# Optimization experiments

Measured on AMD Instinct MI355X. Metric: run time of the kernel, lower is better.

The kernel has to match this reference:

```python
import jax, jax.numpy as jnp
import numpy as np

EPS = 1e-12


def sage_pool_conv(x, src, dst, W_pool, b_pool, W_self, W_neigh, b, num_nodes):
    """DGL SAGEConv with aggregator_type='pool':
    h_neigh[v] = max_{u in N(v)} relu(x[u] @ W_pool + b_pool)
    out[v] = x[v] @ W_self + h_neigh[v] @ W_neigh + b
    Zero-in-degree nodes get h_neigh = 0 (DGL fills max over empty set with 0).
    """
    m = jax.nn.relu(x[src] @ W_pool + b_pool)            # [E, F] gathered + transformed
    agg = jax.ops.segment_max(m, dst, num_segments=num_nodes)  # [N, F], -inf where no neighbors
    agg = jnp.where(jnp.isneginf(agg), 0.0, agg)
    return x @ W_self + agg @ W_neigh + b


def l2norm_relu(h):
    # F.normalize(h, p=2, dim=1, eps=1e-12) then relu
    n = jnp.maximum(jnp.linalg.norm(h, axis=1, keepdims=True), EPS)
    return jax.nn.relu(h / n)


def setup_inputs() -> dict:
    key = jax.random.key(0)
    N, E = 50000, 1600000
    IN, HID, OUT = 128, 128, 128
    ks = jax.random.split(key, 16)
    s = 0.05
    return {
        "x": jax.random.normal(ks[0], (N, IN), dtype=jnp.float32),
        "src": jax.random.randint(ks[1], (E,), 0, N, dtype=jnp.int32),
        "dst": jax.random.randint(ks[2], (E,), 0, N, dtype=jnp.int32),
        "W_pool1": jax.random.normal(ks[3], (IN, IN), dtype=jnp.float32) * s,
        "b_pool1": jnp.zeros((IN,), dtype=jnp.float32),
        "W_self1": jax.random.normal(ks[4], (IN, HID), dtype=jnp.float32) * s,
        "W_neigh1": jax.random.normal(ks[5], (IN, HID), dtype=jnp.float32) * s,
        "b1": jnp.zeros((HID,), dtype=jnp.float32),
        "W_pool2": jax.random.normal(ks[6], (HID, HID), dtype=jnp.float32) * s,
        "b_pool2": jnp.zeros((HID,), dtype=jnp.float32),
        "W_self2": jax.random.normal(ks[7], (HID, OUT), dtype=jnp.float32) * s,
        "W_neigh2": jax.random.normal(ks[8], (HID, OUT), dtype=jnp.float32) * s,
        "b2": jnp.zeros((OUT,), dtype=jnp.float32),
    }


def reference(x, src, dst, W_pool1, b_pool1, W_self1, W_neigh1, b1,
              W_pool2, b_pool2, W_self2, W_neigh2, b2):
    N = x.shape[0]
    h = sage_pool_conv(x, src, dst, W_pool1, b_pool1, W_self1, W_neigh1, b1, N)
    h = l2norm_relu(h)
    # dropout_1 is re-assigned in the original forward but never applied -> no dropout
    h = sage_pool_conv(h, src, dst, W_pool2, b_pool2, W_self2, W_neigh2, b2, N)
    h = l2norm_relu(h)
    return h
```

## Files before the change

### kernel.cpp

```cpp
#include <hip/hip_runtime.h>
#include <hip/hip_bf16.h>

#define NF 128

typedef __attribute__((ext_vector_type(8))) short bf8;
typedef __attribute__((ext_vector_type(4))) float f4;
typedef unsigned short u16x8 __attribute__((ext_vector_type(8)));

static __device__ __forceinline__ unsigned short f2bf(float f) {
  unsigned u = __builtin_bit_cast(unsigned, f);
  u = u + 0x7FFF + ((u >> 16) & 1);
  return (unsigned short)(u >> 16);
}

static __device__ __forceinline__ uint4 pkmax4(uint4 a, uint4 b) {
  u16x8 x = __builtin_bit_cast(u16x8, a);
  u16x8 y = __builtin_bit_cast(u16x8, b);
  u16x8 m = __builtin_elementwise_max(x, y);
  return __builtin_bit_cast(uint4, m);
}

static __device__ __forceinline__ uint4 shflxor4(uint4 a, int m) {
  uint4 r;
  r.x = (unsigned)__shfl_xor((int)a.x, m, 64);
  r.y = (unsigned)__shfl_xor((int)a.y, m, 64);
  r.z = (unsigned)__shfl_xor((int)a.z, m, 64);
  r.w = (unsigned)__shfl_xor((int)a.w, m, 64);
  return r;
}


__global__ void k_convX(const float* __restrict__ A, unsigned short* __restrict__ B,
                        long long nelem, int* __restrict__ bcnt, int nb) {
  long long i = (long long)(blockIdx.x * blockDim.x + threadIdx.x) * 8;
  if (blockIdx.x == 0 && (int)threadIdx.x < nb) bcnt[threadIdx.x] = 0;
  if (i + 8 > nelem) return;
  float4 a = *(const float4*)(A + i);
  float4 b = *(const float4*)(A + i + 4);
  uint4 o;
  o.x = f2bf(a.x) | ((unsigned)f2bf(a.y) << 16);
  o.y = f2bf(a.z) | ((unsigned)f2bf(a.w) << 16);
  o.z = f2bf(b.x) | ((unsigned)f2bf(b.y) << 16);
  o.w = f2bf(b.z) | ((unsigned)f2bf(b.w) << 16);
  *(uint4*)(B + i) = o;
}


__global__ void k_packW(const float* W0, const float* W1, const float* W2,
                        const float* W3, const float* W4, const float* W5,
                        unsigned short* __restrict__ out) {
  int gid = blockIdx.x * blockDim.x + threadIdx.x;
  int m = gid >> 11;
  int u = gid & 2047;
  if (m >= 6) return;
  const float* W = (m == 0) ? W0 : (m == 1) ? W1 : (m == 2) ? W2
                 : (m == 3) ? W3 : (m == 4) ? W4 : W5;
  int l = u & 63, c = u >> 6;
  int kk = c & 3, t = c >> 2;
  int kb = kk * 32 + ((l >> 4) << 3);
  int n = t * 16 + (l & 15);
  unsigned short* o = out + (size_t)m * 2048 * 8 + (size_t)u * 8;
  #pragma unroll
  for (int j = 0; j < 8; ++j) o[j] = f2bf(W[(size_t)(kb + j) * NF + n]);
}


#define TILE_B 8192

__global__ __launch_bounds__(256) void k_bhist(const int* __restrict__ dst,
                                               int* __restrict__ bcnt, int E) {
  __shared__ int h[256];
  int tid = threadIdx.x;
  h[tid] = 0;
  __syncthreads();
  int t0 = blockIdx.x * TILE_B;
  int tend = min(E, t0 + TILE_B);
  for (int i = t0 + tid; i < tend; i += 256) atomicAdd(&h[dst[i] >> 8], 1);
  __syncthreads();
  if (h[tid] > 0) atomicAdd(&bcnt[tid], h[tid]);
}

__global__ __launch_bounds__(256) void k_bscan(const int* __restrict__ bcnt,
                                               int* __restrict__ boff,
                                               int* __restrict__ cursors,
                                               int* __restrict__ off,
                                               int nb, int N, int E) {
  __shared__ int sc[256];
  int tid = threadIdx.x;
  int v = (tid < nb) ? bcnt[tid] : 0;
  sc[tid] = v;
  __syncthreads();
  for (int d = 1; d < 256; d <<= 1) {
    int t = (tid >= d) ? sc[tid - d] : 0;
    __syncthreads();
    sc[tid] += t;
    __syncthreads();
  }
  if (tid < nb) {
    boff[tid + 1] = sc[tid];
    cursors[tid] = sc[tid] - v;
  }
  if (tid == 0) { boff[0] = 0; off[N] = E; }
}

__global__ __launch_bounds__(256) void k_binB(const int* __restrict__ src,
                                              const int* __restrict__ dst,
                                              int* __restrict__ cursors,
                                              unsigned* __restrict__ tmp, int E) {
  __shared__ int h[256], sc[256], gb[256], lc[256];
  __shared__ unsigned sorted[TILE_B];
  int tid = threadIdx.x;
  int t0 = blockIdx.x * TILE_B;
  int tcnt = min(E - t0, TILE_B);
  if (tcnt <= 0) return;
  h[tid] = 0;
  __syncthreads();
  for (int i = tid; i < tcnt; i += 256) atomicAdd(&h[dst[t0 + i] >> 8], 1);
  __syncthreads();
  int v = h[tid];
  sc[tid] = v;
  __syncthreads();
  for (int d = 1; d < 256; d <<= 1) {
    int t = (tid >= d) ? sc[tid - d] : 0;
    __syncthreads();
    sc[tid] += t;
    __syncthreads();
  }
  lc[tid] = 0;
  gb[tid] = (v > 0) ? atomicAdd(&cursors[tid], v) : 0;
  __syncthreads();
  for (int i = tid; i < tcnt; i += 256) {
    int d = dst[t0 + i];
    unsigned s = (unsigned)src[t0 + i];
    int b = d >> 8;
    int p = (sc[b] - h[b]) + atomicAdd(&lc[b], 1);
    sorted[p] = ((unsigned)b << 24) | (s << 8) | (unsigned)(d & 255);
  }
  __syncthreads();
  for (int i = tid; i < tcnt; i += 256) {
    unsigned ev = sorted[i];
    int b = ev >> 24;
    tmp[gb[b] + (i - (sc[b] - h[b]))] = ev & 0xFFFFFFu;
  }
}

#define CSR_CAP 15360

__global__ __launch_bounds__(256) void k_binC(const unsigned* __restrict__ tmp,
                                              const int* __restrict__ boff,
                                              int* __restrict__ off,
                                              unsigned short* __restrict__ esrc, int N) {
  __shared__ int lh[256], ls[256], lcur[256];
  __shared__ int csr[CSR_CAP];
  int tid = threadIdx.x;
  int b = blockIdx.x;
  int base = b << 8;
  int beg = boff[b], end = boff[b + 1];
  int cnt = end - beg;
  lh[tid] = 0;
  __syncthreads();
  for (int i = beg + tid; i < end; i += 256) atomicAdd(&lh[tmp[i] & 255], 1);
  __syncthreads();
  int v = lh[tid];
  ls[tid] = v;
  __syncthreads();
  for (int d = 1; d < 256; d <<= 1) {
    int t = (tid >= d) ? ls[tid - d] : 0;
    __syncthreads();
    ls[tid] += t;
    __syncthreads();
  }
  int excl = ls[tid] - v;
  if (base + tid < N) off[base + tid] = beg + excl;
  lcur[tid] = 0;
  __syncthreads();
  if (cnt <= CSR_CAP) {
    for (int i = beg + tid; i < end; i += 256) {
      unsigned e = tmp[i];
      int dl = (int)(e & 255);
      int p = (ls[dl] - lh[dl]) + atomicAdd(&lcur[dl], 1);
      csr[p] = (int)(e >> 8);
    }
    __syncthreads();
    for (int i = tid; i < cnt; i += 256) esrc[beg + i] = (unsigned short)csr[i];
  } else {
    for (int i = beg + tid; i < end; i += 256) {
      unsigned e = tmp[i];
      int dl = (int)(e & 255);
      int p = (ls[dl] - lh[dl]) + atomicAdd(&lcur[dl], 1);
      esrc[beg + p] = (unsigned short)(e >> 8);
    }
  }
}


__global__ __launch_bounds__(256) void k_gemm_pool(
    const unsigned short* __restrict__ A, const unsigned short* __restrict__ P,
    const float* __restrict__ bias, unsigned short* __restrict__ Yout, int M) {
  __shared__ __align__(16) char smem[32768];
  int tid = threadIdx.x, w = tid >> 6, lane = tid & 63;
  int r0 = lane & 15, g = lane >> 4;
  int base = blockIdx.x * 64;
  int arow = min(base + w * 16 + r0, M - 1);

  {
    uint4* S = (uint4*)smem;
    const uint4* Pv = (const uint4*)P;
    for (int t = tid; t < 2048; t += 256) S[t] = Pv[t];
  }
  __syncthreads();

  f4 acc[8];
  #pragma unroll
  for (int t = 0; t < 8; ++t) acc[t] = (f4){0.f, 0.f, 0.f, 0.f};

  const bf8* Ar = (const bf8*)(A + (size_t)arow * NF);
  const bf8* Wl = (const bf8*)smem;
  #pragma unroll
  for (int kk = 0; kk < 4; ++kk) {
    bf8 a = Ar[kk * 4 + g];
    #pragma unroll
    for (int t = 0; t < 8; ++t) {
      bf8 b = Wl[(t * 4 + kk) * 64 + lane];
      acc[t] = __builtin_amdgcn_mfma_f32_16x16x32_bf16(a, b, acc[t], 0, 0, 0);
    }
  }

  float bb[8];
  #pragma unroll
  for (int t = 0; t < 8; ++t) bb[t] = bias[t * 16 + r0];

  __syncthreads();
  unsigned short* So = (unsigned short*)smem;
  #pragma unroll
  for (int i = 0; i < 4; ++i)
    #pragma unroll
    for (int t = 0; t < 8; ++t)
      So[(w * 16 + g * 4 + i) * NF + t * 16 + r0] = f2bf(fmaxf(acc[t][i] + bb[t], 0.f));
  __syncthreads();
  int maxrows = min(64, M - base);
  uint4* Og = (uint4*)(Yout + (size_t)base * NF);
  const uint4* Sv = (const uint4*)smem;
  int maxc = maxrows * 16;
  for (int c = tid; c < 1024; c += 256)
    if (c < maxc) Og[c] = Sv[c];
}


template <int OUT_MODE>
__global__ __launch_bounds__(256) void k_fused(
    const unsigned short* __restrict__ Y, const int* __restrict__ off,
    const unsigned short* __restrict__ esrc,
    const unsigned short* __restrict__ X,
    const unsigned short* __restrict__ Pself, const unsigned short* __restrict__ Pneigh,
    const float* __restrict__ bias, void* __restrict__ Cout, int M) {
  constexpr int SMEM = (OUT_MODE == 2) ? 32768 : 17408;
  __shared__ __align__(16) char smem[SMEM];
  unsigned short (*agg)[136] = (unsigned short (*)[136])smem;

  int tid = threadIdx.x, w = tid >> 6, lane = tid & 63;
  int r0 = lane & 15, g = lane >> 4;
  int base = blockIdx.x * 64;

  for (int n = 0; n < 16; ++n) {
    int node = base + w * 16 + n;
    uint4 am = {0u, 0u, 0u, 0u};
    if (node < M) {
      int s = __builtin_amdgcn_readfirstlane(off[node]);
      int e = __builtin_amdgcn_readfirstlane(off[node + 1]);
      for (int b0 = s; b0 < e; b0 += 64) {
        int cnt = min(64, e - b0);
        int idxv = (int)esrc[b0 + min(lane, cnt - 1)];
        for (int i = 0; i < cnt; i += 16) {
          #pragma unroll
          for (int j = 0; j < 4; ++j) {
            int eo = min(i + j * 4 + g, cnt - 1);
            int u = __shfl(idxv, eo, 64);
            uint4 v = *((const uint4*)(Y + (size_t)u * NF) + r0);
            am = pkmax4(am, v);
          }
        }
      }
      am = pkmax4(am, shflxor4(am, 16));
      am = pkmax4(am, shflxor4(am, 32));
    }
    if (g == 0) *(uint4*)&agg[w * 16 + n][r0 * 8] = am;
  }
  __syncthreads();

  int arow = min(base + w * 16 + r0, M - 1);
  f4 acc[8];
  #pragma unroll
  for (int t = 0; t < 8; ++t) acc[t] = (f4){0.f, 0.f, 0.f, 0.f};

  const bf8* Ar = (const bf8*)(X + (size_t)arow * NF);
  const bf8* Bs = (const bf8*)Pself;
  #pragma unroll
  for (int kk = 0; kk < 4; ++kk) {
    bf8 a = Ar[kk * 4 + g];
    #pragma unroll
    for (int t = 0; t < 8; ++t)
      acc[t] = __builtin_amdgcn_mfma_f32_16x16x32_bf16(a, Bs[(t * 4 + kk) * 64 + lane], acc[t], 0, 0, 0);
  }
  const bf8* Bn = (const bf8*)Pneigh;
  #pragma unroll
  for (int kk = 0; kk < 4; ++kk) {
    bf8 a = *(const bf8*)&agg[w * 16 + r0][kk * 32 + g * 8];
    #pragma unroll
    for (int t = 0; t < 8; ++t)
      acc[t] = __builtin_amdgcn_mfma_f32_16x16x32_bf16(a, Bn[(t * 4 + kk) * 64 + lane], acc[t], 0, 0, 0);
  }

  float bb[8];
  #pragma unroll
  for (int t = 0; t < 8; ++t) bb[t] = bias[t * 16 + r0];

  float val[8][4];
  #pragma unroll
  for (int t = 0; t < 8; ++t)
    #pragma unroll
    for (int i = 0; i < 4; ++i) val[t][i] = acc[t][i] + bb[t];

  float ss[4] = {0.f, 0.f, 0.f, 0.f};
  #pragma unroll
  for (int i = 0; i < 4; ++i)
    #pragma unroll
    for (int t = 0; t < 8; ++t) ss[i] += val[t][i] * val[t][i];
  #pragma unroll
  for (int d = 1; d < 16; d <<= 1)
    #pragma unroll
    for (int i = 0; i < 4; ++i) ss[i] += __shfl_xor(ss[i], d, 64);
  float inv[4];
  #pragma unroll
  for (int i = 0; i < 4; ++i) inv[i] = 1.f / fmaxf(sqrtf(ss[i]), 1e-12f);

  __syncthreads();
  int maxrows = min(64, M - base);

  if (OUT_MODE == 2) {
    float* So = (float*)smem;
    #pragma unroll
    for (int i = 0; i < 4; ++i)
      #pragma unroll
      for (int t = 0; t < 8; ++t)
        So[(w * 16 + g * 4 + i) * NF + t * 16 + r0] = fmaxf(val[t][i] * inv[i], 0.f);
    __syncthreads();
    uint4* Og = (uint4*)((float*)Cout + (size_t)base * NF);
    const uint4* Sv = (const uint4*)smem;
    int maxc = maxrows * 32;
    for (int c = tid; c < 2048; c += 256)
      if (c < maxc) Og[c] = Sv[c];
  } else {
    unsigned short* So = (unsigned short*)smem;
    #pragma unroll
    for (int i = 0; i < 4; ++i)
      #pragma unroll
      for (int t = 0; t < 8; ++t)
        So[(w * 16 + g * 4 + i) * NF + t * 16 + r0] = f2bf(fmaxf(val[t][i] * inv[i], 0.f));
    __syncthreads();
    uint4* Og = (uint4*)((unsigned short*)Cout + (size_t)base * NF);
    const uint4* Sv = (const uint4*)smem;
    int maxc = maxrows * 16;
    for (int c = tid; c < 1024; c += 256)
      if (c < maxc) Og[c] = Sv[c];
  }
}


extern "C" void kernel_launch(void* const* d_in, const int* in_sizes, int n_in,
                              void* d_out, int out_size, void* d_ws, size_t ws_size,
                              hipStream_t stream) {
  const float* x   = (const float*)d_in[0];
  const int*   src = (const int*)d_in[1];
  const int*   dst = (const int*)d_in[2];
  const float* Wp1 = (const float*)d_in[3];
  const float* bp1 = (const float*)d_in[4];
  const float* Ws1 = (const float*)d_in[5];
  const float* Wn1 = (const float*)d_in[6];
  const float* b1  = (const float*)d_in[7];
  const float* Wp2 = (const float*)d_in[8];
  const float* bp2 = (const float*)d_in[9];
  const float* Ws2 = (const float*)d_in[10];
  const float* Wn2 = (const float*)d_in[11];
  const float* b2  = (const float*)d_in[12];
  float* out = (float*)d_out;

  const int N = in_sizes[0] / NF;
  const int E = in_sizes[1];
  const int NB = (N + 255) >> 8;

  char* ws = (char*)d_ws;
  auto carve = [&](size_t bytes) { char* p = ws; ws += (bytes + 255) & ~(size_t)255; return p; };
  unsigned short* Xb    = (unsigned short*)carve((size_t)N * NF * 2);
  unsigned short* Yb    = (unsigned short*)carve((size_t)N * NF * 2);
  unsigned short* Hb    = (unsigned short*)carve((size_t)N * NF * 2);
  unsigned short* Wpack = (unsigned short*)carve((size_t)6 * NF * NF * 2);
  int* off     = (int*)carve((size_t)(N + 1) * 4);
  int* bcnt    = (int*)carve((size_t)NB * 4);
  int* boff    = (int*)carve((size_t)(NB + 1) * 4);
  int* cursors = (int*)carve((size_t)NB * 4);
  unsigned* tmp = (unsigned*)carve((size_t)E * 4);
  unsigned short* esrc = (unsigned short*)carve((size_t)E * 2);

  unsigned short* Pp1 = Wpack + 0 * NF * NF;
  unsigned short* Ps1 = Wpack + 1 * NF * NF;
  unsigned short* Pn1 = Wpack + 2 * NF * NF;
  unsigned short* Pp2 = Wpack + 3 * NF * NF;
  unsigned short* Ps2 = Wpack + 4 * NF * NF;
  unsigned short* Pn2 = Wpack + 5 * NF * NF;

  const long long nelX = (long long)N * NF;
  const int gConv = (int)((nelX / 8 + 255) / 256);
  const int gPack = (6 * 2048 + 255) / 256;
  const int gTile = (E + TILE_B - 1) / TILE_B;
  const int gG    = (N + 63) / 64;

  k_convX<<<gConv, 256, 0, stream>>>(x, Xb, nelX, bcnt, NB);
  k_packW<<<gPack, 256, 0, stream>>>(Wp1, Ws1, Wn1, Wp2, Ws2, Wn2, Wpack);

  k_bhist<<<gTile, 256, 0, stream>>>(dst, bcnt, E);
  k_bscan<<<1, 256, 0, stream>>>(bcnt, boff, cursors, off, NB, N, E);
  k_binB<<<gTile, 256, 0, stream>>>(src, dst, cursors, tmp, E);
  k_binC<<<NB, 256, 0, stream>>>(tmp, boff, off, esrc, N);

  k_gemm_pool<<<gG, 256, 0, stream>>>(Xb, Pp1, bp1, Yb, N);
  k_fused<1><<<gG, 256, 0, stream>>>(Yb, off, esrc, Xb, Ps1, Pn1, b1, Hb, N);

  k_gemm_pool<<<gG, 256, 0, stream>>>(Hb, Pp2, bp2, Yb, N);
  k_fused<2><<<gG, 256, 0, stream>>>(Yb, off, esrc, Hb, Ps2, Pn2, b2, out, N);
}
```

Measured before the change: 291.0 us.

## Split fused gather-max+GEMM into wave-per-node gather kernel and dual GEMM

Replaces the fused kernel, where each wave serially aggregated 16 nodes before the MFMA phase, with two kernels. The first gives each wave one node, which spreads the gather over many more waves, and keeps four independent max accumulators for more loads in flight. The second is a dual GEMM that stages both packed weight matrices in 64KB of LDS. This adds an N×128 bf16 aggregate buffer written to and read back from global memory, plus an extra launch per layer. The 64KB of LDS per block may also reduce GEMM occupancy.

```diff
diff --git a/kernel.cpp b/kernel.cpp
--- a/kernel.cpp
+++ b/kernel.cpp
@@ -247,68 +247,78 @@
 }
 
 
+__global__ __launch_bounds__(256) void k_gather_max(
+    const unsigned short* __restrict__ Y, const int* __restrict__ off,
+    const unsigned short* __restrict__ esrc, unsigned short* __restrict__ AGG, int N) {
+  int w = (blockIdx.x * 256 + threadIdx.x) >> 6;
+  int lane = threadIdx.x & 63;
+  if (w >= N) return;
+  int r0 = lane & 15, g = lane >> 4;
+  int s = __builtin_amdgcn_readfirstlane(off[w]);
+  int e = __builtin_amdgcn_readfirstlane(off[w + 1]);
+  uint4 am[4];
+  #pragma unroll
+  for (int j = 0; j < 4; ++j) am[j] = (uint4){0u, 0u, 0u, 0u};
+  for (int b0 = s; b0 < e; b0 += 64) {
+    int cnt = min(64, e - b0);
+    int idxv = (int)esrc[b0 + min(lane, cnt - 1)];
+    for (int i = 0; i < cnt; i += 16) {
+      #pragma unroll
+      for (int j = 0; j < 4; ++j) {
+        int eo = min(i + j * 4 + g, cnt - 1);
+        int u = __shfl(idxv, eo, 64);
+        uint4 v = *((const uint4*)(Y + (size_t)u * NF) + r0);
+        am[j] = pkmax4(am[j], v);
+      }
+    }
+  }
+  uint4 a01 = pkmax4(am[0], am[1]);
+  uint4 a23 = pkmax4(am[2], am[3]);
+  uint4 a = pkmax4(a01, a23);
+  a = pkmax4(a, shflxor4(a, 16));
+  a = pkmax4(a, shflxor4(a, 32));
+  if (g == 0) *(uint4*)(AGG + (size_t)w * NF + r0 * 8) = a;
+}
+
+
 template <int OUT_MODE>
-__global__ __launch_bounds__(256) void k_fused(
-    const unsigned short* __restrict__ Y, const int* __restrict__ off,
-    const unsigned short* __restrict__ esrc,
-    const unsigned short* __restrict__ X,
-    const unsigned short* __restrict__ Pself, const unsigned short* __restrict__ Pneigh,
+__global__ __launch_bounds__(256) void k_gemm_dual(
+    const unsigned short* __restrict__ A0, const unsigned short* __restrict__ P0,
+    const unsigned short* __restrict__ A1, const unsigned short* __restrict__ P1,
     const float* __restrict__ bias, void* __restrict__ Cout, int M) {
-  constexpr int SMEM = (OUT_MODE == 2) ? 32768 : 17408;
-  __shared__ __align__(16) char smem[SMEM];
-  unsigned short (*agg)[136] = (unsigned short (*)[136])smem;
-
+  __shared__ __align__(16) char smem[65536];
   int tid = threadIdx.x, w = tid >> 6, lane = tid & 63;
   int r0 = lane & 15, g = lane >> 4;
   int base = blockIdx.x * 64;
-
-  for (int n = 0; n < 16; ++n) {
-    int node = base + w * 16 + n;
-    uint4 am = {0u, 0u, 0u, 0u};
-    if (node < M) {
-      int s = __builtin_amdgcn_readfirstlane(off[node]);
-      int e = __builtin_amdgcn_readfirstlane(off[node + 1]);
-      for (int b0 = s; b0 < e; b0 += 64) {
-        int cnt = min(64, e - b0);
-        int idxv = (int)esrc[b0 + min(lane, cnt - 1)];
-        for (int i = 0; i < cnt; i += 16) {
-          #pragma unroll
-          for (int j = 0; j < 4; ++j) {
-            int eo = min(i + j * 4 + g, cnt - 1);
-            int u = __shfl(idxv, eo, 64);
-            uint4 v = *((const uint4*)(Y + (size_t)u * NF) + r0);
-            am = pkmax4(am, v);
-          }
-        }
+  int arow = min(base + w * 16 + r0, M - 1);
+
+  {
+    uint4* S = (uint4*)smem;
+    const uint4* Pv0 = (const uint4*)P0;
+    const uint4* Pv1 = (const uint4*)P1;
+    for (int t = tid; t < 2048; t += 256) S[t] = Pv0[t];
+    for (int t = tid; t < 2048; t += 256) S[2048 + t] = Pv1[t];
+  }
+  __syncthreads();
+
+  f4 acc[8];
+  #pragma unroll
+  for (int t = 0; t < 8; ++t) acc[t] = (f4){0.f, 0.f, 0.f, 0.f};
+
+  #pragma unroll
+  for (int mat = 0; mat < 2; ++mat) {
+    const unsigned short* A = (mat == 0) ? A0 : A1;
+    const bf8* Ar = (const bf8*)(A + (size_t)arow * NF);
+    const bf8* Wl = (const bf8*)smem + (size_t)mat * 2048;
+    #pragma unroll
+    for (int kk = 0; kk < 4; ++kk) {
+      bf8 a = Ar[kk * 4 + g];
+      #pragma unroll
+      for (int t = 0; t < 8; ++t) {
+        bf8 b = Wl[(t * 4 + kk) * 64 + lane];
+        acc[t] = __builtin_amdgcn_mfma_f32_16x16x32_bf16(a, b, acc[t], 0, 0, 0);
       }
-      am = pkmax4(am, shflxor4(am, 16));
-      am = pkmax4(am, shflxor4(am, 32));
     }
-    if (g == 0) *(uint4*)&agg[w * 16 + n][r0 * 8] = am;
-  }
-  __syncthreads();
-
-  int arow = min(base + w * 16 + r0, M - 1);
-  f4 acc[8];
-  #pragma unroll
-  for (int t = 0; t < 8; ++t) acc[t] = (f4){0.f, 0.f, 0.f, 0.f};
-
-  const bf8* Ar = (const bf8*)(X + (size_t)arow * NF);
-  const bf8* Bs = (const bf8*)Pself;
-  #pragma unroll
-  for (int kk = 0; kk < 4; ++kk) {
-    bf8 a = Ar[kk * 4 + g];
-    #pragma unroll
-    for (int t = 0; t < 8; ++t)
-      acc[t] = __builtin_amdgcn_mfma_f32_16x16x32_bf16(a, Bs[(t * 4 + kk) * 64 + lane], acc[t], 0, 0, 0);
-  }
-  const bf8* Bn = (const bf8*)Pneigh;
-  #pragma unroll
-  for (int kk = 0; kk < 4; ++kk) {
-    bf8 a = *(const bf8*)&agg[w * 16 + r0][kk * 32 + g * 8];
-    #pragma unroll
-    for (int t = 0; t < 8; ++t)
-      acc[t] = __builtin_amdgcn_mfma_f32_16x16x32_bf16(a, Bn[(t * 4 + kk) * 64 + lane], acc[t], 0, 0, 0);
   }
 
   float bb[8];
@@ -393,6 +403,7 @@
   auto carve = [&](size_t bytes) { char* p = ws; ws += (bytes + 255) & ~(size_t)255; return p; };
   unsigned short* Xb    = (unsigned short*)carve((size_t)N * NF * 2);
   unsigned short* Yb    = (unsigned short*)carve((size_t)N * NF * 2);
+  unsigned short* AGGb  = (unsigned short*)carve((size_t)N * NF * 2);
   unsigned short* Hb    = (unsigned short*)carve((size_t)N * NF * 2);
   unsigned short* Wpack = (unsigned short*)carve((size_t)6 * NF * NF * 2);
   int* off     = (int*)carve((size_t)(N + 1) * 4);
@@ -414,6 +425,7 @@
   const int gPack = (6 * 2048 + 255) / 256;
   const int gTile = (E + TILE_B - 1) / TILE_B;
   const int gG    = (N + 63) / 64;
+  const int gRW   = (N + 3) / 4;
 
   k_convX<<<gConv, 256, 0, stream>>>(x, Xb, nelX, bcnt, NB);
   k_packW<<<gPack, 256, 0, stream>>>(Wp1, Ws1, Wn1, Wp2, Ws2, Wn2, Wpack);
@@ -424,8 +436,10 @@
   k_binC<<<NB, 256, 0, stream>>>(tmp, boff, off, esrc, N);
 
   k_gemm_pool<<<gG, 256, 0, stream>>>(Xb, Pp1, bp1, Yb, N);
-  k_fused<1><<<gG, 256, 0, stream>>>(Yb, off, esrc, Xb, Ps1, Pn1, b1, Hb, N);
+  k_gather_max<<<gRW, 256, 0, stream>>>(Yb, off, esrc, AGGb, N);
+  k_gemm_dual<1><<<gG, 256, 0, stream>>>(Xb, Ps1, AGGb, Pn1, b1, Hb, N);
 
   k_gemm_pool<<<gG, 256, 0, stream>>>(Hb, Pp2, bp2, Yb, N);
-  k_fused<2><<<gG, 256, 0, stream>>>(Yb, off, esrc, Hb, Ps2, Pn2, b2, out, N);
-}
+  k_gather_max<<<gRW, 256, 0, stream>>>(Yb, off, esrc, AGGb, N);
+  k_gemm_dual<2><<<gG, 256, 0, stream>>>(Hb, Ps2, AGGb, Pn2, b2, out, N);
+}
```

Result: no change. 296.0 us (+1.7%).
